# Kernel tuning notes

Measured on AMD Instinct MI355X. Metric: run time of the kernel, lower is better.

## Reference

```python
import jax, jax.numpy as jnp
import numpy as np

C = 1.0
MIN = 1e-15
PROJ_EPS = 4e-3  # fp32 ball-projection eps (HGCN convention)

def _artanh(x):
    x = jnp.clip(x, -1.0 + 1e-7, 1.0 - 1e-7)
    return 0.5 * jnp.log((1.0 + x) / (1.0 - x))

def _nrm(x):
    return jnp.clip(jnp.sqrt(jnp.sum(x * x, -1, keepdims=True)), MIN)

def proj(x, c=C):
    n = _nrm(x)
    maxn = (1.0 - PROJ_EPS) / jnp.sqrt(c)
    return jnp.where(n > maxn, x / n * maxn, x)

def expmap0(u, c=C):
    sc = jnp.sqrt(c); n = _nrm(u)
    return jnp.tanh(sc * n) * u / (sc * n)

def logmap0(p, c=C):
    sc = jnp.sqrt(c); n = _nrm(p)
    return _artanh(sc * n) * p / (sc * n)

def mobius_add(x, y, c=C):
    x2 = jnp.sum(x * x, -1, keepdims=True)
    y2 = jnp.sum(y * y, -1, keepdims=True)
    xy = jnp.sum(x * y, -1, keepdims=True)
    num = (1.0 + 2.0 * c * xy + c * y2) * x + (1.0 - c * x2) * y
    den = 1.0 + 2.0 * c * xy + c * c * x2 * y2
    return num / jnp.clip(den, MIN)

def logmap(p1, p2, c=C):
    # log at base p1 of p2
    sub = mobius_add(-p1, p2, c)
    sn = _nrm(sub); sc = jnp.sqrt(c)
    lam = jnp.clip(2.0 / (1.0 - c * jnp.sum(p1 * p1, -1, keepdims=True)), MIN)
    return (2.0 / (sc * lam)) * _artanh(sc * sn) * sub / sn

def expmap(u, p, c=C):
    # exp of tangent u at base p
    sc = jnp.sqrt(c); un = _nrm(u)
    lam = jnp.clip(2.0 / (1.0 - c * jnp.sum(p * p, -1, keepdims=True)), MIN)
    second = jnp.tanh(sc * lam * un / 2.0) * u / (sc * un)
    return mobius_add(p, second, c)

def mobius_matvec(M, x, c=C):
    sc = jnp.sqrt(c)
    xn = _nrm(x)
    mx = x @ M.T
    mxn = _nrm(mx)
    res = jnp.tanh(mxn / xn * _artanh(sc * xn)) * mx / (mxn * sc)
    zero = jnp.all(mx == 0.0, -1, keepdims=True)
    return jnp.where(zero, jnp.zeros_like(res), res)

def hyp_linear(x, W, b, c=C):
    res = proj(mobius_matvec(W, x, c), c)
    hb = proj(expmap0(b, c), c)
    return proj(mobius_add(res, hb, c), c)

def setup_inputs() -> dict:
    key = jax.random.key(0)
    ks = jax.random.split(key, 8)
    B, n, s, d = 2048, 1, 16, 64
    pt = lambda k, shp: proj(0.05 * jax.random.normal(k, shp, dtype=jnp.float32))
    return {
        "self_vectors": pt(ks[0], (B, n, d)),
        "ngh_user_vectors": pt(ks[1], (B, s, d)),
        "ngh_entity_vectors": pt(ks[2], (B, n, s, d)),
        "item_embeddings": pt(ks[3], (B, d)),
        "Wr": 0.05 * jax.random.normal(ks[4], (B, n, s, d, d), dtype=jnp.float32),
        "W_ui": 0.05 * jax.random.normal(ks[5], (d, d), dtype=jnp.float32),
        "lin_W": 0.05 * jax.random.normal(ks[6], (d, d), dtype=jnp.float32),
        "lin_b": 0.05 * jax.random.normal(ks[7], (d,), dtype=jnp.float32),
    }

def reference(self_vectors, ngh_user_vectors, ngh_entity_vectors, item_embeddings, Wr, W_ui, lin_W, lin_b):
    B, n, d = self_vectors.shape  # n == 1 for item layer
    s = ngh_user_vectors.shape[1]
    # ---- entity-side attention + aggregation ----
    t_self = logmap0(self_vectors)                      # [B,n,d]
    t_engh = logmap0(ngh_entity_vectors)                # [B,n,s,d]
    sWr = jnp.einsum('bnc,bnsrc->bnsr', t_self, Wr)     # sum(self*Wr, -1)
    att = jax.nn.softmax(jnp.einsum('bnsr,bnsr->bns', sWr, t_engh), axis=-1)[..., None]
    ngh_log = logmap(self_vectors[:, :, None, :], ngh_entity_vectors)  # [B,n,s,d]
    kg_agg = expmap(jnp.sum(att * ngh_log, axis=2), self_vectors)      # [B,n,d]
    # ---- user-side attention + aggregation ----
    iv = item_embeddings[:, None, :]                    # [B,1,d]
    t_item = logmap0(iv)
    t_ungh = logmap0(ngh_user_vectors)
    imW = jnp.einsum('bod,rd->bor', t_item, W_ui)       # [B,1,d]
    u_att = jax.nn.softmax(jnp.sum(imW * t_ungh, -1), axis=-1)[..., None]  # [B,s,1]
    u_log = logmap(iv, ngh_user_vectors)                # [B,s,d]
    user_agg = expmap(jnp.sum(u_att * u_log, axis=1, keepdims=True), iv)   # [B,1,d]
    # ---- 'sum' aggregation + hyperbolic linear + activation ----
    out = mobius_add(mobius_add(self_vectors, kg_agg), user_agg)
    out = hyp_linear(out.reshape(-1, d), lin_W, lin_b).reshape(B, n, d)
    out = expmap0(jnp.tanh(logmap0(out)))
    return out
```

## Files before the change

kernel.cpp:

```cpp
#include <hip/hip_runtime.h>
#include <hip/hip_bf16.h>

#define MINV 1e-15f
#define MAXNRM 0.996f

__device__ __forceinline__ float wsum(float v) {
#pragma unroll
    for (int m = 32; m; m >>= 1) v += __shfl_xor(v, m, 64);
    return v;
}

__device__ __forceinline__ float artanhf_(float x) {
    x = fminf(fmaxf(x, -1.0f + 1e-7f), 1.0f - 1e-7f);
    return 0.5f * logf((1.0f + x) / (1.0f - x));
}

#define MATVEC4(q, d0, v, acc)                                              \
    acc += (q).x * __shfl((v), (d0) + 0, 64)                                \
         + (q).y * __shfl((v), (d0) + 1, 64)                                \
         + (q).z * __shfl((v), (d0) + 2, 64)                                \
         + (q).w * __shfl((v), (d0) + 3, 64);

__global__ __launch_bounds__(256) void kg_agg_kernel(
    const float* __restrict__ self_v,
    const float* __restrict__ user_v,
    const float* __restrict__ ent_v,
    const float* __restrict__ item_e,
    const float* __restrict__ Wr,
    const float* __restrict__ Wui,
    const float* __restrict__ linW,
    const float* __restrict__ linb,
    float* __restrict__ out)
{
    __shared__ float sE[1024];
    __shared__ float stself[64];
    __shared__ float sRaw[16];

    const int b    = blockIdx.x;
    const int tid  = threadIdx.x;
    const int lane = tid & 63;
    const int wv   = tid >> 6;

    for (int i = tid; i < 1024; i += 256)
        sE[i] = ent_v[(size_t)b * 1024 + i];

    float xl = 0.f, x2 = 0.f;
    if (wv == 0) {
        xl = self_v[(size_t)b * 64 + lane];
        x2 = wsum(xl * xl);
        float xn = fmaxf(sqrtf(x2), MINV);
        stself[lane] = artanhf_(xn) / xn * xl;
    }
    __syncthreads();

    {
        const float4* wp = (const float4*)(Wr + (size_t)b * 65536);
        for (int s = wv; s < 16; s += 4) {
            const float4* sp = wp + s * 1024;
            float acc = 0.f;
#pragma unroll
            for (int j = 0; j < 16; ++j) {
                float4 q = sp[j * 64 + lane];
                int r  = j * 4 + (lane >> 4);
                int c0 = (lane & 15) * 4;
                float er = sE[s * 64 + r];
                float dp = q.x * stself[c0 + 0] + q.y * stself[c0 + 1]
                         + q.z * stself[c0 + 2] + q.w * stself[c0 + 3];
                acc += er * dp;
            }
            acc = wsum(acc);
            if (lane == 0) sRaw[s] = acc;
        }
    }
    __syncthreads();
    if (wv != 0) return;

    float att[16];
    float mxl = -1e30f;
    for (int s = 0; s < 16; ++s) {
        float el = sE[s * 64 + lane];
        float e2 = wsum(el * el);
        float en = fmaxf(sqrtf(e2), MINV);
        float lg = artanhf_(en) / en * sRaw[s];
        att[s] = lg;
        mxl = fmaxf(mxl, lg);
    }
    float ssum = 0.f;
    for (int s = 0; s < 16; ++s) { att[s] = expf(att[s] - mxl); ssum += att[s]; }
    float sinv = 1.f / ssum;

    float lam  = fmaxf(2.f / (1.f - x2), MINV);
    float aggl = 0.f;
    for (int s = 0; s < 16; ++s) {
        float el  = sE[s * 64 + lane];
        float e2  = wsum(el * el);
        float dxe = wsum(xl * el);
        float den = fmaxf(1.f - 2.f * dxe + x2 * e2, MINV);
        float subl = ((1.f - 2.f * dxe + e2) * (-xl) + (1.f - x2) * el) / den;
        float sn = fmaxf(sqrtf(wsum(subl * subl)), MINV);
        float coeff = (2.f / lam) * artanhf_(sn) / sn;
        aggl += (att[s] * sinv) * coeff * subl;
    }
    float un   = fmaxf(sqrtf(wsum(aggl * aggl)), MINV);
    float secl = tanhf(lam * un * 0.5f) * aggl / un;
    float ss2  = wsum(secl * secl);
    float xss  = wsum(xl * secl);
    float kgl  = ((1.f + 2.f * xss + ss2) * xl + (1.f - x2) * secl)
               / fmaxf(1.f + 2.f * xss + x2 * ss2, MINV);

    float ivl = item_e[(size_t)b * 64 + lane];
    float i2  = wsum(ivl * ivl);
    float inn = fmaxf(sqrtf(i2), MINV);
    float til = artanhf_(inn) / inn * ivl;

    float imw = 0.f;
    {
        const float4* wq = (const float4*)Wui;
#pragma unroll
        for (int j = 0; j < 16; ++j) {
            float4 q = wq[lane * 16 + j];
            MATVEC4(q, j * 4, til, imw)
        }
    }

    const float* ub = user_v + (size_t)b * 1024;
    float uatt[16];
    float umx = -1e30f;
    for (int s = 0; s < 16; ++s) {
        float ul = ub[s * 64 + lane];
        float u2 = wsum(ul * ul);
        float unr = fmaxf(sqrtf(u2), MINV);
        float lg  = artanhf_(unr) / unr * wsum(imw * ul);
        uatt[s] = lg;
        umx = fmaxf(umx, lg);
    }
    float usum = 0.f;
    for (int s = 0; s < 16; ++s) { uatt[s] = expf(uatt[s] - umx); usum += uatt[s]; }
    float uinv = 1.f / usum;

    float lami  = fmaxf(2.f / (1.f - i2), MINV);
    float uaggl = 0.f;
    for (int s = 0; s < 16; ++s) {
        float ul  = ub[s * 64 + lane];
        float u2  = wsum(ul * ul);
        float dxy = wsum(ivl * ul);
        float den = fmaxf(1.f - 2.f * dxy + i2 * u2, MINV);
        float subl = ((1.f - 2.f * dxy + u2) * (-ivl) + (1.f - i2) * ul) / den;
        float sn = fmaxf(sqrtf(wsum(subl * subl)), MINV);
        float coeff = (2.f / lami) * artanhf_(sn) / sn;
        uaggl += (uatt[s] * uinv) * coeff * subl;
    }
    float uun  = fmaxf(sqrtf(wsum(uaggl * uaggl)), MINV);
    float usec = tanhf(lami * uun * 0.5f) * uaggl / uun;
    float us2  = wsum(usec * usec);
    float uxs  = wsum(ivl * usec);
    float ual  = ((1.f + 2.f * uxs + us2) * ivl + (1.f - i2) * usec)
               / fmaxf(1.f + 2.f * uxs + i2 * us2, MINV);

    float k2 = wsum(kgl * kgl), xk = wsum(xl * kgl);
    float o1 = ((1.f + 2.f * xk + k2) * xl + (1.f - x2) * kgl)
             / fmaxf(1.f + 2.f * xk + x2 * k2, MINV);
    float o12 = wsum(o1 * o1), ua2 = wsum(ual * ual), o1u = wsum(o1 * ual);
    float v   = ((1.f + 2.f * o1u + ua2) * o1 + (1.f - o12) * ual)
              / fmaxf(1.f + 2.f * o1u + o12 * ua2, MINV);

    float v2 = wsum(v * v);
    float vn = fmaxf(sqrtf(v2), MINV);
    float mxv = 0.f;
    {
        const float4* wq = (const float4*)linW;
#pragma unroll
        for (int j = 0; j < 16; ++j) {
            float4 q = wq[lane * 16 + j];
            MATVEC4(q, j * 4, v, mxv)
        }
    }
    float mxn = fmaxf(sqrtf(wsum(mxv * mxv)), MINV);
    float res = tanhf(mxn / vn * artanhf_(vn)) * mxv / mxn;
    if (__ballot(mxv != 0.f) == 0ull) res = 0.f;
    float rn = fmaxf(sqrtf(wsum(res * res)), MINV);
    if (rn > MAXNRM) res = res / rn * MAXNRM;

    float bl = linb[lane];
    float bn = fmaxf(sqrtf(wsum(bl * bl)), MINV);
    float hb = tanhf(bn) * bl / bn;
    float hn = fmaxf(sqrtf(wsum(hb * hb)), MINV);
    if (hn > MAXNRM) hb = hb / hn * MAXNRM;

    float r2 = wsum(res * res), h2 = wsum(hb * hb), rh = wsum(res * hb);
    float o3 = ((1.f + 2.f * rh + h2) * res + (1.f - r2) * hb)
             / fmaxf(1.f + 2.f * rh + r2 * h2, MINV);
    float on = fmaxf(sqrtf(wsum(o3 * o3)), MINV);
    if (on > MAXNRM) o3 = o3 / on * MAXNRM;

    float on2 = fmaxf(sqrtf(wsum(o3 * o3)), MINV);
    float tl  = tanhf(artanhf_(on2) / on2 * o3);
    float tn  = fmaxf(sqrtf(wsum(tl * tl)), MINV);
    float outl = tanhf(tn) * tl / tn;

    out[(size_t)b * 64 + lane] = outl;
}

extern "C" void kernel_launch(void* const* d_in, const int* in_sizes, int n_in,
                              void* d_out, int out_size, void* d_ws, size_t ws_size,
                              hipStream_t stream) {
    const float* self_v = (const float*)d_in[0];
    const float* user_v = (const float*)d_in[1];
    const float* ent_v  = (const float*)d_in[2];
    const float* item_e = (const float*)d_in[3];
    const float* Wr     = (const float*)d_in[4];
    const float* Wui    = (const float*)d_in[5];
    const float* linW   = (const float*)d_in[6];
    const float* linb   = (const float*)d_in[7];
    float* out = (float*)d_out;

    const int B = in_sizes[0] / 64;
    kg_agg_kernel<<<B, 256, 0, stream>>>(self_v, user_v, ent_v, item_e,
                                         Wr, Wui, linW, linb, out);
}
```

Measured before the change: 732.0 us.

## Split into Wr logits kernel and a wave-parallel tail kernel

The fused kernel becomes two kernels. The first streams Wr and computes the entity attention logits. It accumulates q*e into four accumulators and applies the self tangent vector once per wave, which removes most of the per-element shared-memory reads. The second kernel spreads the per-neighbor logmap and norm work for both entity and user sides across all four waves. It also precomputes the bias projection and the Wui matvec on separate waves before a single wave does the softmax and final transforms. The logits go through the output buffer as scratch, which costs an extra launch and a global round-trip but frees the Wr-streaming kernel from holding long serial tail work.

```diff
diff --git a/kernel.cpp b/kernel.cpp
--- a/kernel.cpp
+++ b/kernel.cpp
@@ -1,5 +1,4 @@
 #include <hip/hip_runtime.h>
-#include <hip/hip_bf16.h>
 
 #define MINV 1e-15f
 #define MAXNRM 0.996f
@@ -21,141 +20,164 @@
          + (q).z * __shfl((v), (d0) + 2, 64)                                \
          + (q).w * __shfl((v), (d0) + 3, 64);
 
-__global__ __launch_bounds__(256) void kg_agg_kernel(
+__global__ __launch_bounds__(256) void logits_kernel(
+    const float* __restrict__ self_v,
+    const float* __restrict__ ent_v,
+    const float* __restrict__ Wr,
+    float* __restrict__ scratch)
+{
+    __shared__ float sE[1024];
+    __shared__ float st[64];
+    const int b = blockIdx.x, tid = threadIdx.x, lane = tid & 63, wv = tid >> 6;
+
+    for (int i = tid; i < 1024; i += 256)
+        sE[i] = ent_v[(size_t)b * 1024 + i];
+    if (wv == 0) {
+        float xl = self_v[(size_t)b * 64 + lane];
+        float x2 = wsum(xl * xl);
+        float xn = fmaxf(sqrtf(x2), MINV);
+        st[lane] = artanhf_(xn) / xn * xl;
+    }
+    __syncthreads();
+
+    const float4* wp = (const float4*)(Wr + (size_t)b * 65536);
+    const int r0 = lane >> 4;
+    const int c0 = (lane & 15) * 4;
+    const float t0 = st[c0], t1 = st[c0 + 1], t2 = st[c0 + 2], t3 = st[c0 + 3];
+
+    for (int s = wv; s < 16; s += 4) {
+        const float4* sp = wp + s * 1024;
+        float ax = 0.f, ay = 0.f, az = 0.f, aw = 0.f;
+#pragma unroll
+        for (int j = 0; j < 16; ++j) {
+            float4 q = sp[j * 64 + lane];
+            float er = sE[s * 64 + j * 4 + r0];
+            ax += q.x * er; ay += q.y * er; az += q.z * er; aw += q.w * er;
+        }
+        float dp = wsum(ax * t0 + ay * t1 + az * t2 + aw * t3);
+        if (lane == 0) scratch[(size_t)b * 64 + s] = dp;
+    }
+}
+
+__global__ __launch_bounds__(256) void tail_kernel(
     const float* __restrict__ self_v,
     const float* __restrict__ user_v,
     const float* __restrict__ ent_v,
     const float* __restrict__ item_e,
-    const float* __restrict__ Wr,
     const float* __restrict__ Wui,
     const float* __restrict__ linW,
     const float* __restrict__ linb,
     float* __restrict__ out)
 {
-    __shared__ float sE[1024];
-    __shared__ float stself[64];
-    __shared__ float sRaw[16];
-
-    const int b    = blockIdx.x;
-    const int tid  = threadIdx.x;
-    const int lane = tid & 63;
-    const int wv   = tid >> 6;
-
-    for (int i = tid; i < 1024; i += 256)
+    __shared__ float sE[1024], sU[1024];
+    __shared__ float sSub[16][64];
+    __shared__ float sUSub[16][64];
+    __shared__ float sLog[16], sULog[16];
+    __shared__ float sImw[64];
+    __shared__ float sHb[64];
+    __shared__ float sH2;
+
+    const int b = blockIdx.x, tid = threadIdx.x, lane = tid & 63, wv = tid >> 6;
+
+    for (int i = tid; i < 1024; i += 256) {
         sE[i] = ent_v[(size_t)b * 1024 + i];
-
-    float xl = 0.f, x2 = 0.f;
-    if (wv == 0) {
-        xl = self_v[(size_t)b * 64 + lane];
-        x2 = wsum(xl * xl);
-        float xn = fmaxf(sqrtf(x2), MINV);
-        stself[lane] = artanhf_(xn) / xn * xl;
-    }
-    __syncthreads();
-
-    {
-        const float4* wp = (const float4*)(Wr + (size_t)b * 65536);
-        for (int s = wv; s < 16; s += 4) {
-            const float4* sp = wp + s * 1024;
-            float acc = 0.f;
-#pragma unroll
-            for (int j = 0; j < 16; ++j) {
-                float4 q = sp[j * 64 + lane];
-                int r  = j * 4 + (lane >> 4);
-                int c0 = (lane & 15) * 4;
-                float er = sE[s * 64 + r];
-                float dp = q.x * stself[c0 + 0] + q.y * stself[c0 + 1]
-                         + q.z * stself[c0 + 2] + q.w * stself[c0 + 3];
-                acc += er * dp;
-            }
-            acc = wsum(acc);
-            if (lane == 0) sRaw[s] = acc;
-        }
-    }
-    __syncthreads();
-    if (wv != 0) return;
-
-    float att[16];
-    float mxl = -1e30f;
-    for (int s = 0; s < 16; ++s) {
-        float el = sE[s * 64 + lane];
-        float e2 = wsum(el * el);
-        float en = fmaxf(sqrtf(e2), MINV);
-        float lg = artanhf_(en) / en * sRaw[s];
-        att[s] = lg;
-        mxl = fmaxf(mxl, lg);
-    }
-    float ssum = 0.f;
-    for (int s = 0; s < 16; ++s) { att[s] = expf(att[s] - mxl); ssum += att[s]; }
-    float sinv = 1.f / ssum;
-
-    float lam  = fmaxf(2.f / (1.f - x2), MINV);
-    float aggl = 0.f;
-    for (int s = 0; s < 16; ++s) {
-        float el  = sE[s * 64 + lane];
-        float e2  = wsum(el * el);
-        float dxe = wsum(xl * el);
-        float den = fmaxf(1.f - 2.f * dxe + x2 * e2, MINV);
-        float subl = ((1.f - 2.f * dxe + e2) * (-xl) + (1.f - x2) * el) / den;
-        float sn = fmaxf(sqrtf(wsum(subl * subl)), MINV);
-        float coeff = (2.f / lam) * artanhf_(sn) / sn;
-        aggl += (att[s] * sinv) * coeff * subl;
-    }
-    float un   = fmaxf(sqrtf(wsum(aggl * aggl)), MINV);
-    float secl = tanhf(lam * un * 0.5f) * aggl / un;
-    float ss2  = wsum(secl * secl);
-    float xss  = wsum(xl * secl);
-    float kgl  = ((1.f + 2.f * xss + ss2) * xl + (1.f - x2) * secl)
-               / fmaxf(1.f + 2.f * xss + x2 * ss2, MINV);
-
-    float ivl = item_e[(size_t)b * 64 + lane];
-    float i2  = wsum(ivl * ivl);
-    float inn = fmaxf(sqrtf(i2), MINV);
-    float til = artanhf_(inn) / inn * ivl;
-
-    float imw = 0.f;
-    {
+        sU[i] = user_v[(size_t)b * 1024 + i];
+    }
+
+    const float xl = self_v[(size_t)b * 64 + lane];
+    const float x2 = wsum(xl * xl);
+    const float ivl = item_e[(size_t)b * 64 + lane];
+    const float i2 = wsum(ivl * ivl);
+
+    if (wv == 3) {
+        float inn = fmaxf(sqrtf(i2), MINV);
+        float til = artanhf_(inn) / inn * ivl;
+        float imw = 0.f;
         const float4* wq = (const float4*)Wui;
 #pragma unroll
         for (int j = 0; j < 16; ++j) {
             float4 q = wq[lane * 16 + j];
             MATVEC4(q, j * 4, til, imw)
         }
-    }
-
-    const float* ub = user_v + (size_t)b * 1024;
-    float uatt[16];
-    float umx = -1e30f;
+        sImw[lane] = imw;
+    } else if (wv == 2) {
+        float bl = linb[lane];
+        float bn = fmaxf(sqrtf(wsum(bl * bl)), MINV);
+        float hb = tanhf(bn) * bl / bn;
+        float hn = fmaxf(sqrtf(wsum(hb * hb)), MINV);
+        if (hn > MAXNRM) hb = hb / hn * MAXNRM;
+        sHb[lane] = hb;
+        float h2 = wsum(hb * hb);
+        if (lane == 0) sH2 = h2;
+    }
+    __syncthreads();
+
+    {
+        const float imw = sImw[lane];
+        const float omx2 = 1.f - x2;
+        const float omi2 = 1.f - i2;
+#pragma unroll
+        for (int q = 0; q < 4; ++q) {
+            const int s = wv * 4 + q;
+            float el = sE[s * 64 + lane];
+            float ul = sU[s * 64 + lane];
+            float e2  = wsum(el * el);
+            float dxe = wsum(xl * el);
+            float u2  = wsum(ul * ul);
+            float dxy = wsum(ivl * ul);
+            float ur  = wsum(imw * ul);
+
+            float en = fmaxf(sqrtf(e2), MINV);
+            if (lane == 0)
+                sLog[s] = artanhf_(en) / en * out[(size_t)b * 64 + s];
+            float den  = fmaxf(1.f - 2.f * dxe + x2 * e2, MINV);
+            float subl = ((1.f - 2.f * dxe + e2) * (-xl) + omx2 * el) / den;
+
+            float unr = fmaxf(sqrtf(u2), MINV);
+            if (lane == 0)
+                sULog[s] = artanhf_(unr) / unr * ur;
+            float uden = fmaxf(1.f - 2.f * dxy + i2 * u2, MINV);
+            float usub = ((1.f - 2.f * dxy + u2) * (-ivl) + omi2 * ul) / uden;
+
+            float sn  = fmaxf(sqrtf(wsum(subl * subl)), MINV);
+            float usn = fmaxf(sqrtf(wsum(usub * usub)), MINV);
+            sSub[s][lane]  = artanhf_(sn) / sn * subl;
+            sUSub[s][lane] = artanhf_(usn) / usn * usub;
+        }
+    }
+    __syncthreads();
+    if (wv != 0) return;
+
+    float mx = -1e30f, umx = -1e30f;
+#pragma unroll
     for (int s = 0; s < 16; ++s) {
-        float ul = ub[s * 64 + lane];
-        float u2 = wsum(ul * ul);
-        float unr = fmaxf(sqrtf(u2), MINV);
-        float lg  = artanhf_(unr) / unr * wsum(imw * ul);
-        uatt[s] = lg;
-        umx = fmaxf(umx, lg);
-    }
-    float usum = 0.f;
-    for (int s = 0; s < 16; ++s) { uatt[s] = expf(uatt[s] - umx); usum += uatt[s]; }
-    float uinv = 1.f / usum;
-
-    float lami  = fmaxf(2.f / (1.f - i2), MINV);
-    float uaggl = 0.f;
+        mx = fmaxf(mx, sLog[s]);
+        umx = fmaxf(umx, sULog[s]);
+    }
+    float se = 0.f, usum = 0.f, aggl = 0.f, uaggl = 0.f;
+#pragma unroll
     for (int s = 0; s < 16; ++s) {
-        float ul  = ub[s * 64 + lane];
-        float u2  = wsum(ul * ul);
-        float dxy = wsum(ivl * ul);
-        float den = fmaxf(1.f - 2.f * dxy + i2 * u2, MINV);
-        float subl = ((1.f - 2.f * dxy + u2) * (-ivl) + (1.f - i2) * ul) / den;
-        float sn = fmaxf(sqrtf(wsum(subl * subl)), MINV);
-        float coeff = (2.f / lami) * artanhf_(sn) / sn;
-        uaggl += (uatt[s] * uinv) * coeff * subl;
-    }
-    float uun  = fmaxf(sqrtf(wsum(uaggl * uaggl)), MINV);
+        float e = expf(sLog[s] - mx);
+        se += e; aggl += e * sSub[s][lane];
+        float ue = expf(sULog[s] - umx);
+        usum += ue; uaggl += ue * sUSub[s][lane];
+    }
+    float lam  = fmaxf(2.f / (1.f - x2), MINV);
+    float lami = fmaxf(2.f / (1.f - i2), MINV);
+    aggl  *= (2.f / lam) / se;
+    uaggl *= (2.f / lami) / usum;
+
+    float un  = fmaxf(sqrtf(wsum(aggl * aggl)), MINV);
+    float uun = fmaxf(sqrtf(wsum(uaggl * uaggl)), MINV);
+    float secl = tanhf(lam * un * 0.5f) * aggl / un;
     float usec = tanhf(lami * uun * 0.5f) * uaggl / uun;
-    float us2  = wsum(usec * usec);
-    float uxs  = wsum(ivl * usec);
-    float ual  = ((1.f + 2.f * uxs + us2) * ivl + (1.f - i2) * usec)
-               / fmaxf(1.f + 2.f * uxs + i2 * us2, MINV);
+
+    float ss2 = wsum(secl * secl), xss = wsum(xl * secl);
+    float us2 = wsum(usec * usec), uxs = wsum(ivl * usec);
+    float kgl = ((1.f + 2.f * xss + ss2) * xl + (1.f - x2) * secl)
+              / fmaxf(1.f + 2.f * xss + x2 * ss2, MINV);
+    float ual = ((1.f + 2.f * uxs + us2) * ivl + (1.f - i2) * usec)
+              / fmaxf(1.f + 2.f * uxs + i2 * us2, MINV);
 
     float k2 = wsum(kgl * kgl), xk = wsum(xl * kgl);
     float o1 = ((1.f + 2.f * xk + k2) * xl + (1.f - x2) * kgl)
@@ -181,13 +203,9 @@
     float rn = fmaxf(sqrtf(wsum(res * res)), MINV);
     if (rn > MAXNRM) res = res / rn * MAXNRM;
 
-    float bl = linb[lane];
-    float bn = fmaxf(sqrtf(wsum(bl * bl)), MINV);
-    float hb = tanhf(bn) * bl / bn;
-    float hn = fmaxf(sqrtf(wsum(hb * hb)), MINV);
-    if (hn > MAXNRM) hb = hb / hn * MAXNRM;
-
-    float r2 = wsum(res * res), h2 = wsum(hb * hb), rh = wsum(res * hb);
+    float hb = sHb[lane];
+    float h2 = sH2;
+    float r2 = wsum(res * res), rh = wsum(res * hb);
     float o3 = ((1.f + 2.f * rh + h2) * res + (1.f - r2) * hb)
              / fmaxf(1.f + 2.f * rh + r2 * h2, MINV);
     float on = fmaxf(sqrtf(wsum(o3 * o3)), MINV);
@@ -196,9 +214,7 @@
     float on2 = fmaxf(sqrtf(wsum(o3 * o3)), MINV);
     float tl  = tanhf(artanhf_(on2) / on2 * o3);
     float tn  = fmaxf(sqrtf(wsum(tl * tl)), MINV);
-    float outl = tanhf(tn) * tl / tn;
-
-    out[(size_t)b * 64 + lane] = outl;
+    out[(size_t)b * 64 + lane] = tanhf(tn) * tl / tn;
 }
 
 extern "C" void kernel_launch(void* const* d_in, const int* in_sizes, int n_in,
@@ -215,6 +231,8 @@
     float* out = (float*)d_out;
 
     const int B = in_sizes[0] / 64;
-    kg_agg_kernel<<<B, 256, 0, stream>>>(self_v, user_v, ent_v, item_e,
-                                         Wr, Wui, linW, linb, out);
-}
+
+    logits_kernel<<<B, 256, 0, stream>>>(self_v, ent_v, Wr, out);
+    tail_kernel<<<B, 256, 0, stream>>>(self_v, user_v, ent_v, item_e,
+                                       Wui, linW, linb, out);
+}
```

Result: no change. 725.9 us (-0.8%).
